# Performance work log

Hardware: AMD Instinct MI355X
Metric: run time of the kernel (lower is better)

## Reference

```python
import jax, jax.numpy as jnp
import numpy as np

N = 100_000   # nodes
E = 600_000   # edges per layer (avg degree ~6, ogbn-arxiv-like)
IN, H, C = 128, 256, 40


def _sage_layer(x, src, dst, w_self, w_neigh, b):
    """DGL SAGEConv with mean aggregator: fc_self(x) + fc_neigh(mean_nbr) + b."""
    n = x.shape[0]
    msg = x[src]                                               # [E, d] gather
    agg = jax.ops.segment_sum(msg, dst, num_segments=n)        # [N, d]
    deg = jax.ops.segment_sum(jnp.ones((src.shape[0],), x.dtype), dst,
                              num_segments=n)                  # [N]
    h_neigh = agg / jnp.maximum(deg, 1.0)[:, None]             # mean; 0 if isolated
    return x @ w_self.T + h_neigh @ w_neigh.T + b


def setup_inputs() -> dict:
    key = jax.random.key(0)
    ks = jax.random.split(key, 11)
    s = 0.02
    return {
        "x": jax.random.normal(ks[0], (N, IN), jnp.float32),
        "src1": jax.random.randint(ks[1], (E,), 0, N, jnp.int32),
        "dst1": jax.random.randint(ks[2], (E,), 0, N, jnp.int32),
        "src2": jax.random.randint(ks[3], (E,), 0, N, jnp.int32),
        "dst2": jax.random.randint(ks[4], (E,), 0, N, jnp.int32),
        "w_self1": s * jax.random.normal(ks[5], (H, IN), jnp.float32),
        "w_neigh1": s * jax.random.normal(ks[6], (H, IN), jnp.float32),
        "b1": jnp.zeros((H,), jnp.float32),
        "w_self2": s * jax.random.normal(ks[7], (C, H), jnp.float32),
        "w_neigh2": s * jax.random.normal(ks[8], (C, H), jnp.float32),
        "b2": jnp.zeros((C,), jnp.float32),
    }


def reference(x, src1, dst1, src2, dst2, w_self1, w_neigh1, b1,
              w_self2, w_neigh2, b2):
    h = jax.nn.relu(_sage_layer(x, src1, dst1, w_self1, w_neigh1, b1))
    return _sage_layer(h, src2, dst2, w_self2, w_neigh2, b2)
```

## Files before the change

kernel.cpp:

```cpp
#include <hip/hip_runtime.h>
#include <hip/hip_bf16.h>
#include <cstdint>
#include <cstddef>


#define D_IN 128
#define D_H  256
#define D_C  40

#define NBLK     128
#define NBKT_MAX 392
#define BKT_CAP  2560

typedef __bf16 bf16_t;
typedef __attribute__((ext_vector_type(8))) __bf16 bf16x8;
typedef __attribute__((ext_vector_type(4))) __bf16 bf16x4;
typedef __attribute__((ext_vector_type(4))) float  f32x4;

static constexpr size_t NMAX = 100000;
static constexpr size_t EMAX = 600000;
static constexpr size_t NSC_MAX = (size_t)NBKT_MAX * NBLK;
static constexpr size_t alignup(size_t v) { return (v + 255) & ~size_t(255); }

static constexpr size_t HG1_OFF  = 0;
static constexpr size_t HG2_OFF  = alignup(HG1_OFF + NSC_MAX * 4);
static constexpr size_t BS1_OFF  = alignup(HG2_OFF + NSC_MAX * 4);
static constexpr size_t BS2_OFF  = alignup(BS1_OFF + 512 * 4);
static constexpr size_t RP1_OFF  = alignup(BS2_OFF + 512 * 4);
static constexpr size_t RP2_OFF  = alignup(RP1_OFF + (NMAX + 1) * 4);
static constexpr size_t BKT1_OFF = alignup(RP2_OFF + (NMAX + 1) * 4);
static constexpr size_t BKT2_OFF = alignup(BKT1_OFF + EMAX * 4);
static constexpr size_t XCAT_OFF = alignup(BKT2_OFF + EMAX * 4);
static constexpr size_t P_OFF    = alignup(XCAT_OFF + (NMAX + 128) * 256 * 2);
static constexpr size_t W1F_OFF  = alignup(P_OFF + NMAX * 40 * 2);
static constexpr size_t W2F_OFF  = alignup(W1F_OFF + 32 * 256 * 8 * 2);
static constexpr size_t WS_NEEDED = W2F_OFF + 32 * 80 * 8 * 2;

__global__ __launch_bounds__(256) void k_prep(
    const float* __restrict__ x, bf16_t* __restrict__ xcat,
    const float* __restrict__ ws1, const float* __restrict__ wn1,
    const float* __restrict__ ws2, const float* __restrict__ wn2,
    bf16_t* __restrict__ w1f, bf16_t* __restrict__ w2f,
    const int* __restrict__ dst1, const int* __restrict__ dst2,
    int* __restrict__ hg1, int* __restrict__ hg2,
    int N, int E, int chunk, int nbkt, int nconvx) {
  __shared__ int h[NBKT_MAX];
  int bid = blockIdx.x;

  if (bid < nconvx) {
    int t = bid * 256 + threadIdx.x;
    if (t < N * 16) {
      int row = t >> 4, j = t & 15;
      const float* sp = x + (size_t)row * 128 + j * 8;
      float4 v0 = ((const float4*)sp)[0];
      float4 v1 = ((const float4*)sp)[1];
      bf16x8 o;
      o[0] = (bf16_t)v0.x; o[1] = (bf16_t)v0.y; o[2] = (bf16_t)v0.z; o[3] = (bf16_t)v0.w;
      o[4] = (bf16_t)v1.x; o[5] = (bf16_t)v1.y; o[6] = (bf16_t)v1.z; o[7] = (bf16_t)v1.w;
      *(bf16x8*)(xcat + (size_t)row * 256 + j * 8) = o;
    }
    return;
  }
  bid -= nconvx;

  if (bid < 32) {
    int t = bid * 256 + threadIdx.x;
    {
      int ks4g = t >> 8, col = t & 255;
      int k0 = (ks4g >> 2) * 32 + (ks4g & 3) * 8;
      bf16x8 o;
#pragma unroll
      for (int i = 0; i < 8; ++i) {
        int k = k0 + i;
        float v = (k < 128) ? ws1[col * 128 + k] : wn1[col * 128 + (k - 128)];
        o[i] = (bf16_t)v;
      }
      *(bf16x8*)(w1f + (size_t)t * 8) = o;
    }
    if (t < 32 * 80) {
      int ks4g = t / 80, col = t - ks4g * 80;
      int k0 = (ks4g >> 2) * 32 + (ks4g & 3) * 8;
      bf16x8 o;
#pragma unroll
      for (int i = 0; i < 8; ++i) {
        int k = k0 + i;
        float v = (col < 40) ? ws2[col * 256 + k] : wn2[(col - 40) * 256 + k];
        o[i] = (bf16_t)v;
      }
      *(bf16x8*)(w2f + (size_t)t * 8) = o;
    }
    return;
  }
  bid -= 32;
  {
    const int* dst = (bid >> 7) ? dst2 : dst1;
    int*       hg  = (bid >> 7) ? hg2 : hg1;
    int        cb  = bid & 127;
    for (int i = threadIdx.x; i < nbkt; i += 256) h[i] = 0;
    __syncthreads();
    int beg = cb * chunk, end = min(E, beg + chunk);
    for (int e = beg + threadIdx.x; e < end; e += 256)
      atomicAdd(&h[dst[e] >> 8], 1);
    __syncthreads();
    for (int b = threadIdx.x; b < nbkt; b += 256)
      hg[b * NBLK + cb] = h[b];
  }
}

__global__ void k_scan_block(int* __restrict__ a1, int* __restrict__ a2,
                             int* __restrict__ b1s, int* __restrict__ b2s, int n) {
  int* a    = blockIdx.y ? a2 : a1;
  int* bsum = blockIdx.y ? b2s : b1s;
  __shared__ int lds[256];
  int t = threadIdx.x, i = blockIdx.x * 256 + t;
  int v = (i < n) ? a[i] : 0;
  lds[t] = v;
  __syncthreads();
  for (int off = 1; off < 256; off <<= 1) {
    int add = (t >= off) ? lds[t - off] : 0;
    __syncthreads();
    lds[t] += add;
    __syncthreads();
  }
  if (i < n) a[i] = lds[t] - v;
  if (t == 255) bsum[blockIdx.x] = lds[255];
}

__global__ void k_scan_sums(int* __restrict__ b1s, int* __restrict__ b2s, int nb) {
  int* bsum = blockIdx.x ? b2s : b1s;
  __shared__ int lds[512];
  int t = threadIdx.x;
  int v = (t < nb) ? bsum[t] : 0;
  lds[t] = v;
  __syncthreads();
  for (int off = 1; off < 512; off <<= 1) {
    int add = (t >= off) ? lds[t - off] : 0;
    __syncthreads();
    lds[t] += add;
    __syncthreads();
  }
  if (t < nb) bsum[t] = lds[t] - v;
}

__global__ void k_scan_add(int* __restrict__ a1, int* __restrict__ a2,
                           const int* __restrict__ b1s, const int* __restrict__ b2s, int n) {
  int* a        = blockIdx.y ? a2 : a1;
  const int* bs = blockIdx.y ? b2s : b1s;
  int i = blockIdx.x * 256 + threadIdx.x;
  if (i < n) a[i] += bs[i >> 8];
}

__global__ void k_scat(const int* __restrict__ src1, const int* __restrict__ dst1,
                       const int* __restrict__ src2, const int* __restrict__ dst2,
                       const int* __restrict__ off1, const int* __restrict__ off2,
                       unsigned* __restrict__ bkt1, unsigned* __restrict__ bkt2,
                       int E, int chunk, int nbkt) {
  const int* src = blockIdx.y ? src2 : src1;
  const int* dst = blockIdx.y ? dst2 : dst1;
  const int* off = blockIdx.y ? off2 : off1;
  unsigned*  bkt = blockIdx.y ? bkt2 : bkt1;
  __shared__ int cur[NBKT_MAX];
  for (int i = threadIdx.x; i < nbkt; i += 256)
    cur[i] = off[i * NBLK + blockIdx.x];
  __syncthreads();
  int beg = blockIdx.x * chunk, end = min(E, beg + chunk);
  for (int e = beg + threadIdx.x; e < end; e += 256) {
    int d = dst[e];
    int slot = atomicAdd(&cur[d >> 8], 1);
    bkt[slot] = (unsigned)src[e] | ((unsigned)(d & 255) << 24);
  }
}

__global__ __launch_bounds__(256) void k_bcsr(
    const int* __restrict__ off1, const int* __restrict__ off2,
    const unsigned* bkt1, const unsigned* bkt2,
    int* csr1, int* csr2,
    int* __restrict__ rp1, int* __restrict__ rp2, int E, int N, int nbkt) {
  const int* off      = blockIdx.y ? off2 : off1;
  const unsigned* bkt = blockIdx.y ? bkt2 : bkt1;
  int* csr            = blockIdx.y ? csr2 : csr1;
  int* rowptr         = blockIdx.y ? rp2 : rp1;

  const int b = blockIdx.x, t = threadIdx.x;
  const int base = off[b * NBLK];
  const int endp = (b == nbkt - 1) ? E : off[(b + 1) * NBLK];
  const int cnt  = endp - base;

  __shared__ int hist[256];
  __shared__ int sc[256];
  __shared__ int cur[256];
  __shared__ int stage[BKT_CAP];

  hist[t] = 0;
  __syncthreads();
  for (int i = t; i < cnt; i += 256)
    atomicAdd(&hist[bkt[base + i] >> 24], 1);
  __syncthreads();

  int v = hist[t];
  sc[t] = v;
  __syncthreads();
  for (int off_ = 1; off_ < 256; off_ <<= 1) {
    int add = (t >= off_) ? sc[t - off_] : 0;
    __syncthreads();
    sc[t] += add;
    __syncthreads();
  }
  int excl = sc[t] - v;

  int node = b * 256 + t;
  if (node < N) rowptr[node] = base + excl;
  if (b == nbkt - 1 && t == 0) rowptr[N] = E;
  cur[t] = excl;
  __syncthreads();

  for (int i = t; i < cnt; i += 256) {
    unsigned u = bkt[base + i];
    int slot = atomicAdd(&cur[u >> 24], 1);
    if (slot < BKT_CAP) stage[slot] = (int)(u & 0xFFFFFFu);
  }
  __syncthreads();
  for (int i = t; i < cnt; i += 256)
    csr[base + i] = stage[i];
}

__global__ void k_agg1(bf16_t* __restrict__ xcat, const int* __restrict__ rowptr,
                       const int* __restrict__ csr, int N) {
  int t = blockIdx.x * 256 + threadIdx.x;
  int node = t >> 4, l = t & 15;
  if (node >= N) return;
  int beg = rowptr[node], end = rowptr[node + 1];
  float acc[8] = {0.f, 0.f, 0.f, 0.f, 0.f, 0.f, 0.f, 0.f};
  for (int e = beg; e < end; ++e) {
    int s = csr[e];
    bf16x8 v = *(const bf16x8*)(xcat + (size_t)s * 256 + l * 8);
#pragma unroll
    for (int i = 0; i < 8; ++i) acc[i] += (float)v[i];
  }
  float rd = (end > beg) ? 1.0f / (float)(end - beg) : 0.0f;
  bf16x8 o;
#pragma unroll
  for (int i = 0; i < 8; ++i) o[i] = (bf16_t)(acc[i] * rd);
  *(bf16x8*)(xcat + (size_t)node * 256 + 128 + l * 8) = o;
}

__global__ __launch_bounds__(256, 2) void k_fused(
    const bf16_t* __restrict__ xcat, const bf16_t* __restrict__ w1f,
    const float* __restrict__ b1, const bf16_t* __restrict__ w2f,
    const float* __restrict__ b2v, float* __restrict__ out,
    bf16_t* __restrict__ p, int N) {
  __shared__ __align__(16) char lds[65536];
  const int tid  = (int)threadIdx.x;
  const int wv   = tid >> 6;
  const int lane = tid & 63;
  const int lr   = lane & 15;
  const int lg   = lane >> 4;
  const int c0   = wv * 64;
  const int m0   = (int)blockIdx.x * 128;

  {
    const char* tb = (const char*)(xcat + (size_t)m0 * 256);
#pragma unroll
    for (int i = 0; i < 16; ++i) {
      int L   = i * 4096 + tid * 16;
      int row = L >> 9;
      int c   = L & 511;
      int so  = (row << 9) | (c ^ ((row & 7) << 4));
      __builtin_amdgcn_global_load_lds(
          (const __attribute__((address_space(1))) void*)(tb + so),
          (__attribute__((address_space(3))) void*)(lds + L), 16, 0, 0);
    }
  }
  __syncthreads();

  f32x4 acc[4][8] = {};
#pragma unroll
  for (int ks = 0; ks < 8; ++ks) {
    bf16x8 wf[4];
#pragma unroll
    for (int wb = 0; wb < 4; ++wb)
      wf[wb] = *(const bf16x8*)(w1f + ((size_t)(ks * 4 + lg) * 256 +
                                       (c0 + wb * 16 + lr)) * 8);
    bf16x8 ax[8];
#pragma unroll
    for (int rb = 0; rb < 8; ++rb) {
      int lrow = rb * 16 + lr;
      ax[rb] = *(const bf16x8*)(lds + lrow * 512 +
                                ((ks * 64 + lg * 16) ^ ((lrow & 7) << 4)));
    }
#pragma unroll
    for (int wb = 0; wb < 4; ++wb)
#pragma unroll
      for (int rb = 0; rb < 8; ++rb)
        acc[wb][rb] = __builtin_amdgcn_mfma_f32_16x16x32_bf16(
            wf[wb], ax[rb], acc[wb][rb], 0, 0, 0);
  }

  __syncthreads();

#pragma unroll
  for (int wb = 0; wb < 4; ++wb) {
    float4 b4 = *(const float4*)(b1 + c0 + wb * 16 + lg * 4);
#pragma unroll
    for (int rb = 0; rb < 8; ++rb) {
      int xrow = rb * 16 + lr;
      bf16x4 o;
      o[0] = (bf16_t)fmaxf(acc[wb][rb][0] + b4.x, 0.f);
      o[1] = (bf16_t)fmaxf(acc[wb][rb][1] + b4.y, 0.f);
      o[2] = (bf16_t)fmaxf(acc[wb][rb][2] + b4.z, 0.f);
      o[3] = (bf16_t)fmaxf(acc[wb][rb][3] + b4.w, 0.f);
      *(bf16x4*)(lds + xrow * 512 +
                 ((c0 * 2 + wb * 32 + lg * 8) ^ ((xrow & 7) << 4))) = o;
    }
  }
  __syncthreads();

  f32x4 acc2[2][5] = {};
#pragma unroll
  for (int ks = 0; ks < 8; ++ks) {
    bf16x8 hf[2];
#pragma unroll
    for (int m = 0; m < 2; ++m) {
      int arow = wv * 32 + m * 16 + lr;
      hf[m] = *(const bf16x8*)(lds + arow * 512 +
                               ((ks * 64 + lg * 16) ^ ((arow & 7) << 4)));
    }
#pragma unroll
    for (int wb = 0; wb < 5; ++wb) {
      bf16x8 w2 = *(const bf16x8*)(w2f + ((size_t)(ks * 4 + lg) * 80 +
                                          (wb * 16 + lr)) * 8);
#pragma unroll
      for (int m = 0; m < 2; ++m)
        acc2[m][wb] = __builtin_amdgcn_mfma_f32_16x16x32_bf16(
            w2, hf[m], acc2[m][wb], 0, 0, 0);
    }
  }

#pragma unroll
  for (int m = 0; m < 2; ++m) {
    const int r = m0 + wv * 32 + m * 16 + lr;
    if (r < N) {
#pragma unroll
      for (int wb = 0; wb < 5; ++wb) {
        int col0 = wb * 16 + lg * 4;
        f32x4 v = acc2[m][wb];
        if (col0 < 40) {
          float4 b4 = *(const float4*)(b2v + col0);
          v[0] += b4.x; v[1] += b4.y; v[2] += b4.z; v[3] += b4.w;
          *(f32x4*)(out + (size_t)r * 40 + col0) = v;
        } else {
          bf16x4 o;
          o[0] = (bf16_t)v[0]; o[1] = (bf16_t)v[1];
          o[2] = (bf16_t)v[2]; o[3] = (bf16_t)v[3];
          *(bf16x4*)(p + (size_t)r * 40 + (col0 - 40)) = o;
        }
      }
    }
  }
}

__global__ void k_agg2fin(const bf16_t* __restrict__ p, const int* __restrict__ rowptr,
                          const int* __restrict__ csr, float* __restrict__ out, int N) {
  int t = blockIdx.x * 256 + threadIdx.x;
  int node = t / 10, l = t - node * 10;
  if (node >= N) return;
  int beg = rowptr[node], end = rowptr[node + 1];
  float a0 = 0.f, a1 = 0.f, a2 = 0.f, a3 = 0.f;
  for (int e = beg; e < end; ++e) {
    int s = csr[e];
    bf16x4 v = *(const bf16x4*)(p + (size_t)s * 40 + l * 4);
    a0 += (float)v[0]; a1 += (float)v[1]; a2 += (float)v[2]; a3 += (float)v[3];
  }
  float rd = (end > beg) ? 1.0f / (float)(end - beg) : 0.0f;
  float* o = out + (size_t)node * 40 + l * 4;
  float4 cur = *(const float4*)o;
  cur.x += a0 * rd;
  cur.y += a1 * rd;
  cur.z += a2 * rd;
  cur.w += a3 * rd;
  *(float4*)o = cur;
}

extern "C" void kernel_launch(void* const* d_in, const int* in_sizes, int n_in,
                              void* d_out, int out_size, void* d_ws, size_t ws_size,
                              hipStream_t stream) {
  const float* x    = (const float*)d_in[0];
  const int*   src1 = (const int*)d_in[1];
  const int*   dst1 = (const int*)d_in[2];
  const int*   src2 = (const int*)d_in[3];
  const int*   dst2 = (const int*)d_in[4];
  const float* ws1  = (const float*)d_in[5];
  const float* wn1  = (const float*)d_in[6];
  const float* b1   = (const float*)d_in[7];
  const float* ws2  = (const float*)d_in[8];
  const float* wn2  = (const float*)d_in[9];
  const float* b2   = (const float*)d_in[10];
  float*       out  = (float*)d_out;

  const int N = in_sizes[0] / D_IN;
  const int E = in_sizes[1];
  if (ws_size < WS_NEEDED) return;

  char*     ws   = (char*)d_ws;
  int*      hg1  = (int*)(ws + HG1_OFF);
  int*      hg2  = (int*)(ws + HG2_OFF);
  int*      bs1  = (int*)(ws + BS1_OFF);
  int*      bs2  = (int*)(ws + BS2_OFF);
  int*      rp1  = (int*)(ws + RP1_OFF);
  int*      rp2  = (int*)(ws + RP2_OFF);
  unsigned* bkt1 = (unsigned*)(ws + BKT1_OFF);
  unsigned* bkt2 = (unsigned*)(ws + BKT2_OFF);
  int*      csr1 = (int*)(ws + BKT1_OFF);
  int*      csr2 = (int*)(ws + BKT2_OFF);
  bf16_t*   xcat = (bf16_t*)(ws + XCAT_OFF);
  bf16_t*   p    = (bf16_t*)(ws + P_OFF);
  bf16_t*   w1f  = (bf16_t*)(ws + W1F_OFF);
  bf16_t*   w2f  = (bf16_t*)(ws + W2F_OFF);

  const int nbkt  = (N + 255) >> 8;
  const int chunk = (E + NBLK - 1) / NBLK;
  const int nsc   = nbkt * NBLK;
  const int nscb  = (nsc + 255) / 256;
  const int nconvx = (N * 16 + 255) / 256;
  const int ntiles = (N + 127) / 128;

  k_prep<<<nconvx + 32 + 2 * NBLK, 256, 0, stream>>>(
      x, xcat, ws1, wn1, ws2, wn2, w1f, w2f, dst1, dst2, hg1, hg2,
      N, E, chunk, nbkt, nconvx);

  k_scan_block<<<dim3(nscb, 2), 256, 0, stream>>>(hg1, hg2, bs1, bs2, nsc);
  k_scan_sums<<<2, 512, 0, stream>>>(bs1, bs2, nscb);
  k_scan_add<<<dim3(nscb, 2), 256, 0, stream>>>(hg1, hg2, bs1, bs2, nsc);
  k_scat<<<dim3(NBLK, 2), 256, 0, stream>>>(src1, dst1, src2, dst2, hg1, hg2,
                                            bkt1, bkt2, E, chunk, nbkt);
  k_bcsr<<<dim3(nbkt, 2), 256, 0, stream>>>(hg1, hg2, bkt1, bkt2, csr1, csr2,
                                            rp1, rp2, E, N, nbkt);

  k_agg1<<<(N * 16 + 255) / 256, 256, 0, stream>>>(xcat, rp1, csr1, N);
  k_fused<<<ntiles, 256, 0, stream>>>(xcat, w1f, b1, w2f, b2, out, p, N);
  k_agg2fin<<<(N * 10 + 255) / 256, 256, 0, stream>>>(p, rp2, csr2, out, N);
}
```

Measured before the change: 153.0 us.

## Split fused two-GEMM kernel into separate LDS-free GEMM kernels with global hidden buffer

Replaces the fused kernel, which staged the xcat tile in 64KB LDS and kept the hidden layer on-chip, with two kernels. The first computes layer-1 GEMM+bias+ReLU from direct global loads on 64-row tiles and writes a bf16 hidden buffer to global memory. The second reads that buffer for the layer-2 GEMM. The aim is to free LDS and raise occupancy (launch bounds 4), at the cost of a 51MB round trip through HBM for the hidden activations, an extra launch, and uncoalesced direct global A-loads.

```diff
diff --git a/kernel.cpp b/kernel.cpp
--- a/kernel.cpp
+++ b/kernel.cpp
@@ -31,7 +31,8 @@
 static constexpr size_t BKT1_OFF = alignup(RP2_OFF + (NMAX + 1) * 4);
 static constexpr size_t BKT2_OFF = alignup(BKT1_OFF + EMAX * 4);
 static constexpr size_t XCAT_OFF = alignup(BKT2_OFF + EMAX * 4);
-static constexpr size_t P_OFF    = alignup(XCAT_OFF + (NMAX + 128) * 256 * 2);
+static constexpr size_t HB_OFF   = alignup(XCAT_OFF + (NMAX + 128) * 256 * 2);
+static constexpr size_t P_OFF    = alignup(HB_OFF + (NMAX + 128) * 256 * 2);
 static constexpr size_t W1F_OFF  = alignup(P_OFF + NMAX * 40 * 2);
 static constexpr size_t W2F_OFF  = alignup(W1F_OFF + 32 * 256 * 8 * 2);
 static constexpr size_t WS_NEEDED = W2F_OFF + 32 * 80 * 8 * 2;
@@ -244,36 +245,23 @@
   *(bf16x8*)(xcat + (size_t)node * 256 + 128 + l * 8) = o;
 }
 
-__global__ __launch_bounds__(256, 2) void k_fused(
+__global__ __launch_bounds__(256, 4) void k_gemm1(
     const bf16_t* __restrict__ xcat, const bf16_t* __restrict__ w1f,
-    const float* __restrict__ b1, const bf16_t* __restrict__ w2f,
-    const float* __restrict__ b2v, float* __restrict__ out,
-    bf16_t* __restrict__ p, int N) {
-  __shared__ __align__(16) char lds[65536];
+    const float* __restrict__ b1, bf16_t* __restrict__ hb, int N) {
   const int tid  = (int)threadIdx.x;
   const int wv   = tid >> 6;
   const int lane = tid & 63;
   const int lr   = lane & 15;
   const int lg   = lane >> 4;
   const int c0   = wv * 64;
-  const int m0   = (int)blockIdx.x * 128;
-
-  {
-    const char* tb = (const char*)(xcat + (size_t)m0 * 256);
-#pragma unroll
-    for (int i = 0; i < 16; ++i) {
-      int L   = i * 4096 + tid * 16;
-      int row = L >> 9;
-      int c   = L & 511;
-      int so  = (row << 9) | (c ^ ((row & 7) << 4));
-      __builtin_amdgcn_global_load_lds(
-          (const __attribute__((address_space(1))) void*)(tb + so),
-          (__attribute__((address_space(3))) void*)(lds + L), 16, 0, 0);
-    }
-  }
-  __syncthreads();
-
-  f32x4 acc[4][8] = {};
+  const int m0   = (int)blockIdx.x * 64;
+
+  const bf16_t* xrow[4];
+#pragma unroll
+  for (int rb = 0; rb < 4; ++rb)
+    xrow[rb] = xcat + (size_t)(m0 + rb * 16 + lr) * 256 + lg * 8;
+
+  f32x4 acc[4][4] = {};
 #pragma unroll
   for (int ks = 0; ks < 8; ++ks) {
     bf16x8 wf[4];
@@ -281,50 +269,59 @@
     for (int wb = 0; wb < 4; ++wb)
       wf[wb] = *(const bf16x8*)(w1f + ((size_t)(ks * 4 + lg) * 256 +
                                        (c0 + wb * 16 + lr)) * 8);
-    bf16x8 ax[8];
-#pragma unroll
-    for (int rb = 0; rb < 8; ++rb) {
-      int lrow = rb * 16 + lr;
-      ax[rb] = *(const bf16x8*)(lds + lrow * 512 +
-                                ((ks * 64 + lg * 16) ^ ((lrow & 7) << 4)));
-    }
+    bf16x8 ax[4];
+#pragma unroll
+    for (int rb = 0; rb < 4; ++rb)
+      ax[rb] = *(const bf16x8*)(xrow[rb] + ks * 32);
 #pragma unroll
     for (int wb = 0; wb < 4; ++wb)
 #pragma unroll
-      for (int rb = 0; rb < 8; ++rb)
+      for (int rb = 0; rb < 4; ++rb)
         acc[wb][rb] = __builtin_amdgcn_mfma_f32_16x16x32_bf16(
             wf[wb], ax[rb], acc[wb][rb], 0, 0, 0);
   }
 
-  __syncthreads();
-
 #pragma unroll
   for (int wb = 0; wb < 4; ++wb) {
     float4 b4 = *(const float4*)(b1 + c0 + wb * 16 + lg * 4);
 #pragma unroll
-    for (int rb = 0; rb < 8; ++rb) {
-      int xrow = rb * 16 + lr;
-      bf16x4 o;
-      o[0] = (bf16_t)fmaxf(acc[wb][rb][0] + b4.x, 0.f);
-      o[1] = (bf16_t)fmaxf(acc[wb][rb][1] + b4.y, 0.f);
-      o[2] = (bf16_t)fmaxf(acc[wb][rb][2] + b4.z, 0.f);
-      o[3] = (bf16_t)fmaxf(acc[wb][rb][3] + b4.w, 0.f);
-      *(bf16x4*)(lds + xrow * 512 +
-                 ((c0 * 2 + wb * 32 + lg * 8) ^ ((xrow & 7) << 4))) = o;
-    }
-  }
-  __syncthreads();
+    for (int rb = 0; rb < 4; ++rb) {
+      int r = m0 + rb * 16 + lr;
+      if (r < N) {
+        bf16x4 o;
+        o[0] = (bf16_t)fmaxf(acc[wb][rb][0] + b4.x, 0.f);
+        o[1] = (bf16_t)fmaxf(acc[wb][rb][1] + b4.y, 0.f);
+        o[2] = (bf16_t)fmaxf(acc[wb][rb][2] + b4.z, 0.f);
+        o[3] = (bf16_t)fmaxf(acc[wb][rb][3] + b4.w, 0.f);
+        *(bf16x4*)(hb + (size_t)r * 256 + c0 + wb * 16 + lg * 4) = o;
+      }
+    }
+  }
+}
+
+__global__ __launch_bounds__(256, 4) void k_gemm2(
+    const bf16_t* __restrict__ hb, const bf16_t* __restrict__ w2f,
+    const float* __restrict__ b2v, float* __restrict__ out,
+    bf16_t* __restrict__ p, int N) {
+  const int tid  = (int)threadIdx.x;
+  const int wv   = tid >> 6;
+  const int lane = tid & 63;
+  const int lr   = lane & 15;
+  const int lg   = lane >> 4;
+  const int r0   = (int)blockIdx.x * 128 + wv * 32;
+
+  const bf16_t* hrow[2];
+#pragma unroll
+  for (int m = 0; m < 2; ++m)
+    hrow[m] = hb + (size_t)(r0 + m * 16 + lr) * 256 + lg * 8;
 
   f32x4 acc2[2][5] = {};
 #pragma unroll
   for (int ks = 0; ks < 8; ++ks) {
     bf16x8 hf[2];
 #pragma unroll
-    for (int m = 0; m < 2; ++m) {
-      int arow = wv * 32 + m * 16 + lr;
-      hf[m] = *(const bf16x8*)(lds + arow * 512 +
-                               ((ks * 64 + lg * 16) ^ ((arow & 7) << 4)));
-    }
+    for (int m = 0; m < 2; ++m)
+      hf[m] = *(const bf16x8*)(hrow[m] + ks * 32);
 #pragma unroll
     for (int wb = 0; wb < 5; ++wb) {
       bf16x8 w2 = *(const bf16x8*)(w2f + ((size_t)(ks * 4 + lg) * 80 +
@@ -338,7 +335,7 @@
 
 #pragma unroll
   for (int m = 0; m < 2; ++m) {
-    const int r = m0 + wv * 32 + m * 16 + lr;
+    const int r = r0 + m * 16 + lr;
     if (r < N) {
 #pragma unroll
       for (int wb = 0; wb < 5; ++wb) {
@@ -413,6 +410,7 @@
   int*      csr1 = (int*)(ws + BKT1_OFF);
   int*      csr2 = (int*)(ws + BKT2_OFF);
   bf16_t*   xcat = (bf16_t*)(ws + XCAT_OFF);
+  bf16_t*   hbuf = (bf16_t*)(ws + HB_OFF);
   bf16_t*   p    = (bf16_t*)(ws + P_OFF);
   bf16_t*   w1f  = (bf16_t*)(ws + W1F_OFF);
   bf16_t*   w2f  = (bf16_t*)(ws + W2F_OFF);
@@ -422,7 +420,6 @@
   const int nsc   = nbkt * NBLK;
   const int nscb  = (nsc + 255) / 256;
   const int nconvx = (N * 16 + 255) / 256;
-  const int ntiles = (N + 127) / 128;
 
   k_prep<<<nconvx + 32 + 2 * NBLK, 256, 0, stream>>>(
       x, xcat, ws1, wn1, ws2, wn2, w1f, w2f, dst1, dst2, hg1, hg2,
@@ -437,6 +434,7 @@
                                             rp1, rp2, E, N, nbkt);
 
   k_agg1<<<(N * 16 + 255) / 256, 256, 0, stream>>>(xcat, rp1, csr1, N);
-  k_fused<<<ntiles, 256, 0, stream>>>(xcat, w1f, b1, w2f, b2, out, p, N);
+  k_gemm1<<<(N + 63) / 64, 256, 0, stream>>>(xcat, w1f, b1, hbuf, N);
+  k_gemm2<<<(N + 127) / 128, 256, 0, stream>>>(hbuf, w2f, b2, out, p, N);
   k_agg2fin<<<(N * 10 + 255) / 256, 256, 0, stream>>>(p, rp2, csr2, out, N);
 }
```

Result: slower. 184.3 us (+20.5%).

## Retile fused MLP kernel per-wave over 32 rows and all hidden columns

Applied to the files above, without the earlier changes.

Each wave now computes a 32-row by 256-column slice of the first GEMM. It reads its input rows straight from global memory into registers instead of staging a 128-row tile in LDS with global_load_lds. The hidden activations go to a private per-wave LDS region, so the block-wide __syncthreads become a wave-local lgkmcnt wait. In exchange each wave re-reads the full first-layer weight matrix from cache, and the un-unrolled K loop leaves global load latency exposed.

```diff
diff --git a/kernel.cpp b/kernel.cpp
--- a/kernel.cpp
+++ b/kernel.cpp
@@ -255,74 +255,55 @@
   const int lane = tid & 63;
   const int lr   = lane & 15;
   const int lg   = lane >> 4;
-  const int c0   = wv * 64;
-  const int m0   = (int)blockIdx.x * 128;
-
-  {
-    const char* tb = (const char*)(xcat + (size_t)m0 * 256);
-#pragma unroll
-    for (int i = 0; i < 16; ++i) {
-      int L   = i * 4096 + tid * 16;
-      int row = L >> 9;
-      int c   = L & 511;
-      int so  = (row << 9) | (c ^ ((row & 7) << 4));
-      __builtin_amdgcn_global_load_lds(
-          (const __attribute__((address_space(1))) void*)(tb + so),
-          (__attribute__((address_space(3))) void*)(lds + L), 16, 0, 0);
-    }
-  }
-  __syncthreads();
-
-  f32x4 acc[4][8] = {};
-#pragma unroll
+  const int r0   = (int)blockIdx.x * 128 + wv * 32;
+  char* hbuf = lds + wv * 16384;
+
+  const bf16_t* xr0 = xcat + (size_t)(r0 + lr) * 256 + lg * 8;
+  const bf16_t* xr1 = xr0 + 16 * 256;
+  const bf16_t* wb0 = w1f + ((size_t)lg * 256 + lr) * 8;
+
+  f32x4 acc[16][2] = {};
+#pragma unroll 1
   for (int ks = 0; ks < 8; ++ks) {
-    bf16x8 wf[4];
-#pragma unroll
-    for (int wb = 0; wb < 4; ++wb)
-      wf[wb] = *(const bf16x8*)(w1f + ((size_t)(ks * 4 + lg) * 256 +
-                                       (c0 + wb * 16 + lr)) * 8);
-    bf16x8 ax[8];
-#pragma unroll
-    for (int rb = 0; rb < 8; ++rb) {
-      int lrow = rb * 16 + lr;
-      ax[rb] = *(const bf16x8*)(lds + lrow * 512 +
-                                ((ks * 64 + lg * 16) ^ ((lrow & 7) << 4)));
-    }
-#pragma unroll
-    for (int wb = 0; wb < 4; ++wb)
-#pragma unroll
-      for (int rb = 0; rb < 8; ++rb)
-        acc[wb][rb] = __builtin_amdgcn_mfma_f32_16x16x32_bf16(
-            wf[wb], ax[rb], acc[wb][rb], 0, 0, 0);
-  }
-
-  __syncthreads();
-
-#pragma unroll
-  for (int wb = 0; wb < 4; ++wb) {
-    float4 b4 = *(const float4*)(b1 + c0 + wb * 16 + lg * 4);
-#pragma unroll
-    for (int rb = 0; rb < 8; ++rb) {
+    bf16x8 ax0 = *(const bf16x8*)(xr0 + ks * 32);
+    bf16x8 ax1 = *(const bf16x8*)(xr1 + ks * 32);
+    const bf16_t* wk = wb0 + (size_t)ks * (4 * 256 * 8);
+    bf16x8 wf[16];
+#pragma unroll
+    for (int wb = 0; wb < 16; ++wb)
+      wf[wb] = *(const bf16x8*)(wk + wb * (16 * 8));
+#pragma unroll
+    for (int wb = 0; wb < 16; ++wb) {
+      acc[wb][0] = __builtin_amdgcn_mfma_f32_16x16x32_bf16(wf[wb], ax0, acc[wb][0], 0, 0, 0);
+      acc[wb][1] = __builtin_amdgcn_mfma_f32_16x16x32_bf16(wf[wb], ax1, acc[wb][1], 0, 0, 0);
+    }
+  }
+
+#pragma unroll
+  for (int wb = 0; wb < 16; ++wb) {
+    float4 b4 = *(const float4*)(b1 + wb * 16 + lg * 4);
+#pragma unroll
+    for (int rb = 0; rb < 2; ++rb) {
       int xrow = rb * 16 + lr;
       bf16x4 o;
       o[0] = (bf16_t)fmaxf(acc[wb][rb][0] + b4.x, 0.f);
       o[1] = (bf16_t)fmaxf(acc[wb][rb][1] + b4.y, 0.f);
       o[2] = (bf16_t)fmaxf(acc[wb][rb][2] + b4.z, 0.f);
       o[3] = (bf16_t)fmaxf(acc[wb][rb][3] + b4.w, 0.f);
-      *(bf16x4*)(lds + xrow * 512 +
-                 ((c0 * 2 + wb * 32 + lg * 8) ^ ((xrow & 7) << 4))) = o;
-    }
-  }
-  __syncthreads();
+      *(bf16x4*)(hbuf + xrow * 512 + ((wb * 32 + lg * 8) ^ ((xrow & 7) << 4))) = o;
+    }
+  }
+  asm volatile("s_waitcnt lgkmcnt(0)" ::: "memory");
+  __builtin_amdgcn_sched_barrier(0);
 
   f32x4 acc2[2][5] = {};
-#pragma unroll
+#pragma unroll 1
   for (int ks = 0; ks < 8; ++ks) {
     bf16x8 hf[2];
 #pragma unroll
     for (int m = 0; m < 2; ++m) {
-      int arow = wv * 32 + m * 16 + lr;
-      hf[m] = *(const bf16x8*)(lds + arow * 512 +
+      int arow = m * 16 + lr;
+      hf[m] = *(const bf16x8*)(hbuf + arow * 512 +
                                ((ks * 64 + lg * 16) ^ ((arow & 7) << 4)));
     }
 #pragma unroll
@@ -338,7 +319,7 @@
 
 #pragma unroll
   for (int m = 0; m < 2; ++m) {
-    const int r = m0 + wv * 32 + m * 16 + lr;
+    const int r = r0 + m * 16 + lr;
     if (r < N) {
 #pragma unroll
       for (int wb = 0; wb < 5; ++wb) {
@@ -422,7 +403,6 @@
   const int nsc   = nbkt * NBLK;
   const int nscb  = (nsc + 255) / 256;
   const int nconvx = (N * 16 + 255) / 256;
-  const int ntiles = (N + 127) / 128;
 
   k_prep<<<nconvx + 32 + 2 * NBLK, 256, 0, stream>>>(
       x, xcat, ws1, wn1, ws2, wn2, w1f, w2f, dst1, dst2, hg1, hg2,
@@ -437,6 +417,6 @@
                                             rp1, rp2, E, N, nbkt);
 
   k_agg1<<<(N * 16 + 255) / 256, 256, 0, stream>>>(xcat, rp1, csr1, N);
-  k_fused<<<ntiles, 256, 0, stream>>>(xcat, w1f, b1, w2f, b2, out, p, N);
+  k_fused<<<(N + 127) / 128, 256, 0, stream>>>(xcat, w1f, b1, w2f, b2, out, p, N);
   k_agg2fin<<<(N * 10 + 255) / 256, 256, 0, stream>>>(p, rp2, csr2, out, N);
 }
```

Measured after the change: 174.5 us. +14.1%, slower.
